# Kernel optimization log

Hardware: AMD Instinct MI355X
Metric: run time of the kernel (lower is better)

Reference implementation:

```python
import jax, jax.numpy as jnp
import numpy as np

N = 50000      # nodes
E = 800000     # edges
F_IN = 64      # num_node_features
H = 128        # hidden_channels
C = 2          # num_classes
G = 16         # graphs in batch


def setup_inputs() -> dict:
    key = jax.random.key(0)
    ks = jax.random.split(key, 16)
    def lin(k, fan_in, shape):
        return jax.random.normal(k, shape, jnp.float32) / np.sqrt(fan_in)
    return {
        "x": jax.random.normal(ks[0], (N, F_IN), jnp.float32),
        "edge_index": jax.random.randint(ks[1], (2, E), 0, N, dtype=jnp.int32),
        "batch": jnp.sort(jax.random.randint(ks[2], (N,), 0, G, dtype=jnp.int32)),
        "W1": lin(ks[3], F_IN, (F_IN, H)), "b1": jnp.zeros((H,), jnp.float32),
        "W2": lin(ks[4], H, (H, H)),       "b2": jnp.zeros((H,), jnp.float32),
        "W3": lin(ks[5], H, (H, H)),       "b3": jnp.zeros((H,), jnp.float32),
        "W4": lin(ks[6], H, (H, H)),       "b4": jnp.zeros((H,), jnp.float32),
        "lw1": lin(ks[7], H, (H, H // 2)), "lb1": jnp.zeros((H // 2,), jnp.float32),
        "lw2": lin(ks[8], H // 2, (H // 2, C)), "lb2": jnp.zeros((C,), jnp.float32),
    }


def _graph_norm(edge_index):
    # PyG GCNConv default: add self-loops, symmetric normalization.
    loop = jnp.arange(N, dtype=edge_index.dtype)
    src = jnp.concatenate([edge_index[0], loop])  # message source
    dst = jnp.concatenate([edge_index[1], loop])  # aggregation target
    deg = jax.ops.segment_sum(jnp.ones_like(dst, jnp.float32), dst, num_segments=N)
    dinv = jnp.where(deg > 0, jax.lax.rsqrt(deg), 0.0)
    norm = dinv[src] * dinv[dst]                  # [E+N]
    return src, dst, norm


def _gcn_conv(h, W, b, src, dst, norm):
    hw = h @ W                                    # [N, out]
    msg = hw[src] * norm[:, None]                 # gather + normalize  [E+N, out]
    agg = jax.ops.segment_sum(msg, dst, num_segments=N)  # scatter-add
    return agg + b


def reference(x, edge_index, batch, W1, b1, W2, b2, W3, b3, W4, b4, lw1, lb1, lw2, lb2):
    src, dst, norm = _graph_norm(edge_index)
    h = jax.nn.relu(_gcn_conv(x, W1, b1, src, dst, norm))   # dropout inactive (eval)
    h = jax.nn.relu(_gcn_conv(h, W2, b2, src, dst, norm))
    h = jax.nn.relu(_gcn_conv(h, W3, b3, src, dst, norm))
    h = _gcn_conv(h, W4, b4, src, dst, norm)
    # global_mean_pool over graph ids
    cnt = jax.ops.segment_sum(jnp.ones((N,), jnp.float32), batch, num_segments=G)
    pooled = jax.ops.segment_sum(h, batch, num_segments=G) / jnp.maximum(cnt, 1.0)[:, None]
    out = jax.nn.relu(pooled @ lw1 + lb1)
    return out @ lw2 + lb2
```

## Files before the change

### kernel.cpp

```cpp
#include <hip/hip_runtime.h>

#define NN 50000
#define NPAD 50048
#define NE 800000
#define FIN 64
#define H 128
#define NG 16
#define NPART 64
#define NBUCK 196
#define BUCK_CAP 4800
#define FILLA_BLOCKS 512
#define FILLA_CHUNK 1563
#define CHUNK_U 16
#define DUMMY NN
#define AGG_CH (NPAD / 64)
#define ZERO_I4 32768
#define PREP_ITEMS (NPAD * FIN + H * FIN + 3 * H * H + ZERO_I4)
#define PREP_BLOCKS ((PREP_ITEMS + 255) / 256)

typedef __bf16 bf16x8 __attribute__((ext_vector_type(8)));
typedef float f32x4 __attribute__((ext_vector_type(4)));
typedef float f32x2 __attribute__((ext_vector_type(2)));
typedef unsigned int u32x4 __attribute__((ext_vector_type(4)));

__device__ inline unsigned short bf16r(float x) {
    unsigned int u = __float_as_uint(x);
    return (unsigned short)((u + 0x7fffu + ((u >> 16) & 1u)) >> 16);
}
__device__ inline unsigned int pack_bf16x2(float a, float b) {
    return (unsigned int)bf16r(a) | ((unsigned int)bf16r(b) << 16);
}
__device__ inline float bf_lo(unsigned int u) { return __uint_as_float(u << 16); }
__device__ inline float bf_hi(unsigned int u) { return __uint_as_float(u & 0xffff0000u); }

__device__ inline void pkadd(f32x2& a, unsigned int u) {
    f32x2 p;
    p.x = bf_lo(u);
    p.y = bf_hi(u);
    asm("v_pk_add_f32 %0, %1, %0" : "+v"(a) : "v"(p));
}

__global__ __launch_bounds__(256) void fillA_prep_kernel(const int* __restrict__ ei,
                                                         int* __restrict__ gcount,
                                                         unsigned int* __restrict__ ebuf,
                                                         const float* __restrict__ x,
                                                         const float* __restrict__ W1,
                                                         const float* __restrict__ W2,
                                                         const float* __restrict__ W3,
                                                         const float* __restrict__ W4,
                                                         unsigned short* __restrict__ xb,
                                                         unsigned short* __restrict__ Wt1,
                                                         unsigned short* __restrict__ Wt2,
                                                         unsigned short* __restrict__ Wt3,
                                                         unsigned short* __restrict__ Wt4,
                                                         int4* __restrict__ zbuf) {
    const int t = threadIdx.x;
    if (blockIdx.x >= FILLA_BLOCKS) {
        int e = (blockIdx.x - FILLA_BLOCKS) * 256 + t;
        if (e < NPAD * FIN) {
            int n = e >> 6, k = e & 63;
            unsigned short v = (n < NN) ? bf16r(x[n * FIN + k]) : (unsigned short)0;
            xb[(size_t)(k >> 5) * (NPAD * 32) + n * 32 + (k & 31)] = v;
            return;
        }
        int tt = e - NPAD * FIN;
        if (tt < H * FIN) {
            int n = tt / FIN, k = tt % FIN;
            Wt1[tt] = bf16r(W1[k * H + n]);
            return;
        }
        int u = tt - H * FIN;
        if (u < 3 * H * H) {
            const float* W = W2;
            unsigned short* Wt = Wt2;
            if (u >= 2 * H * H) { W = W4; Wt = Wt4; u -= 2 * H * H; }
            else if (u >= H * H) { W = W3; Wt = Wt3; u -= H * H; }
            int n = u / H, k = u % H;
            Wt[u] = bf16r(W[k * H + n]);
            return;
        }
        int z = u - 3 * H * H;
        if (z < ZERO_I4) zbuf[z] = make_int4(0, 0, 0, 0);
        return;
    }
    __shared__ int hist[256];
    __shared__ int base[256];
    hist[t] = 0;
    __syncthreads();
    const int e0 = blockIdx.x * FILLA_CHUNK;
    const int e1 = min(e0 + FILLA_CHUNK, NE);
    for (int e = e0 + t; e < e1; e += 256)
        atomicAdd(&hist[ei[NE + e] >> 8], 1);
    __syncthreads();
    {
        int h = hist[t];
        base[t] = h ? atomicAdd(&gcount[t], h) : 0;
    }
    __syncthreads();
    for (int e = e0 + t; e < e1; e += 256) {
        int d = ei[NE + e];
        int s = ei[e];
        int b = d >> 8;
        int pos = atomicAdd(&base[b], 1);
        ebuf[b * BUCK_CAP + pos] = (unsigned int)s | ((unsigned int)d << 16);
    }
}

__global__ __launch_bounds__(256) void fillB_kernel(const unsigned int* __restrict__ ebuf,
                                                    const int* __restrict__ gcount,
                                                    int* __restrict__ galloc,
                                                    int* __restrict__ pcnt,
                                                    const int* __restrict__ batch,
                                                    int2* __restrict__ rowse,
                                                    float* __restrict__ dinv,
                                                    unsigned short* __restrict__ csr) {
    __shared__ int lh[256];
    __shared__ int lsum[256];
    __shared__ int lcur[256];
    __shared__ int lgc[16];
    __shared__ int base_s;
    const int b = blockIdx.x, t = threadIdx.x;
    const int n0 = b * 256;
    lh[t] = 0;
    if (t < 16) lgc[t] = 0;
    __syncthreads();
    const int ne = gcount[b];
    const unsigned int* __restrict__ eb = ebuf + b * BUCK_CAP;
    for (int i = t; i < ne; i += 256)
        atomicAdd(&lh[(int)(eb[i] >> 16) - n0], 1);
    __syncthreads();
    const int c = lh[t];
    const int p = (c + 7) & ~7;
    const int n = n0 + t;
    if (n < NN) atomicAdd(&lgc[batch[n]], 1);
    lsum[t] = p;
    __syncthreads();
    if (t < 16 && lgc[t]) atomicAdd(&pcnt[t], lgc[t]);
    for (int off = 1; off < 256; off <<= 1) {
        int u = (t >= off) ? lsum[t - off] : 0;
        __syncthreads();
        lsum[t] += u;
        __syncthreads();
    }
    if (t == 255) base_s = atomicAdd(galloc, lsum[255]);
    const int excl = t ? lsum[t - 1] : 0;
    __syncthreads();
    const int st = base_s + excl;
    if (n < NN) {
        rowse[n] = make_int2(st, st + p);
        dinv[n] = rsqrtf((float)c + 1.0f);
    } else if (n < NPAD) {
        rowse[n] = make_int2(0, 0);
        dinv[n] = 0.0f;
    }
    lcur[t] = st;
    __syncthreads();
    for (int i = t; i < ne; i += 256) {
        unsigned int u = eb[i];
        int pos = atomicAdd(&lcur[(int)(u >> 16) - n0], 1);
        csr[pos] = (unsigned short)(u & 0xFFFFu);
    }
    __syncthreads();
    for (int k = st + c; k < st + p; k++) csr[k] = (unsigned short)DUMMY;
}

#define LSTRIDE 130
template <int K>
__global__ __launch_bounds__(256) void gemm_mfma_kernel(const unsigned short* __restrict__ hb,
                                                        const unsigned short* __restrict__ Wt,
                                                        const float* __restrict__ dinv,
                                                        unsigned int* __restrict__ outu) {
    __shared__ float ls[64 * LSTRIDE];
    const int wave = threadIdx.x >> 6, lane = threadIdx.x & 63;
    const int m15 = lane & 15, quad = lane >> 4;
    const int row0 = blockIdx.x * 64;
    const int arow = row0 + wave * 16 + m15;

    bf16x8 a[K / 32];
#pragma unroll
    for (int ks = 0; ks < K / 32; ks++)
        a[ks] = *(const bf16x8*)&hb[(size_t)ks * (NPAD * 32) + arow * 32 + quad * 8];

    const int lrow = wave * 16 + quad * 4;
    float dv[4];
#pragma unroll
    for (int r = 0; r < 4; r++) dv[r] = dinv[row0 + lrow + r];

#pragma unroll
    for (int ct = 0; ct < 8; ct++) {
        f32x4 acc = {0.f, 0.f, 0.f, 0.f};
#pragma unroll
        for (int ks = 0; ks < K / 32; ks++) {
            bf16x8 b = *(const bf16x8*)&Wt[(ct * 16 + m15) * K + ks * 32 + quad * 8];
            acc = __builtin_amdgcn_mfma_f32_16x16x32_bf16(a[ks], b, acc, 0, 0, 0);
        }
#pragma unroll
        for (int r = 0; r < 4; r++)
            ls[(lrow + r) * LSTRIDE + ct * 16 + m15] = acc[r] * dv[r];
    }
    __syncthreads();

#pragma unroll
    for (int k = 0; k < 4; k++) {
        int idx = threadIdx.x + 256 * k;
        int c = idx >> 8, row = (idx >> 2) & 63, q = idx & 3;
        const float* p = &ls[row * LSTRIDE + c * 32 + q * 8];
        uint4 o;
        o.x = pack_bf16x2(p[0], p[1]);
        o.y = pack_bf16x2(p[2], p[3]);
        o.z = pack_bf16x2(p[4], p[5]);
        o.w = pack_bf16x2(p[6], p[7]);
        *(uint4*)&outu[(size_t)c * (NPAD * CHUNK_U) + (size_t)(row0 + row) * CHUNK_U + q * 4] = o;
    }
}

template <int MODE>
__global__ __launch_bounds__(256) void agg_kernel(const unsigned int* __restrict__ hwc,
                                                  const int2* __restrict__ rowse,
                                                  const unsigned short* __restrict__ csr,
                                                  const float* __restrict__ dinv,
                                                  const float* __restrict__ bias,
                                                  const int* __restrict__ batch,
                                                  float* __restrict__ poolpart,
                                                  unsigned int* __restrict__ outc) {
    const int b = blockIdx.x;
    const int chunk = (b & 7) >> 1;
    const int nb = (b >> 3) * 2 + (b & 1);
    const int g = threadIdx.x & 3;
    const int n = nb * 64 + (threadIdx.x >> 2);
    const int u0 = g * 4;
    const unsigned int* __restrict__ slice = hwc + (size_t)chunk * (NPAD * CHUNK_U);

    uint4 sv = *(const uint4*)&slice[n * CHUNK_U + u0];
    f32x2 a0 = {bf_lo(sv.x), bf_hi(sv.x)};
    f32x2 a1 = {bf_lo(sv.y), bf_hi(sv.y)};
    f32x2 a2 = {bf_lo(sv.z), bf_hi(sv.z)};
    f32x2 a3 = {bf_lo(sv.w), bf_hi(sv.w)};

    const int2 se = rowse[n];
    int i = se.x;
    for (; i + 16 <= se.y; i += 16) {
        uint4 c0 = *(const uint4*)&csr[i];
        uint4 c1 = *(const uint4*)&csr[i + 8];
        int s0 = c0.x & 0xFFFF, s1 = c0.x >> 16;
        int s2 = c0.y & 0xFFFF, s3 = c0.y >> 16;
        int s4 = c0.z & 0xFFFF, s5 = c0.z >> 16;
        int s6 = c0.w & 0xFFFF, s7 = c0.w >> 16;
        int t0 = c1.x & 0xFFFF, t1 = c1.x >> 16;
        int t2 = c1.y & 0xFFFF, t3 = c1.y >> 16;
        int t4 = c1.z & 0xFFFF, t5 = c1.z >> 16;
        int t6 = c1.w & 0xFFFF, t7 = c1.w >> 16;
        uint4 v0 = *(const uint4*)&slice[s0 * CHUNK_U + u0];
        uint4 v1 = *(const uint4*)&slice[s1 * CHUNK_U + u0];
        uint4 v2 = *(const uint4*)&slice[s2 * CHUNK_U + u0];
        uint4 v3 = *(const uint4*)&slice[s3 * CHUNK_U + u0];
        uint4 v4 = *(const uint4*)&slice[s4 * CHUNK_U + u0];
        uint4 v5 = *(const uint4*)&slice[s5 * CHUNK_U + u0];
        uint4 v6 = *(const uint4*)&slice[s6 * CHUNK_U + u0];
        uint4 v7 = *(const uint4*)&slice[s7 * CHUNK_U + u0];
        uint4 w0 = *(const uint4*)&slice[t0 * CHUNK_U + u0];
        uint4 w1 = *(const uint4*)&slice[t1 * CHUNK_U + u0];
        uint4 w2 = *(const uint4*)&slice[t2 * CHUNK_U + u0];
        uint4 w3 = *(const uint4*)&slice[t3 * CHUNK_U + u0];
        uint4 w4 = *(const uint4*)&slice[t4 * CHUNK_U + u0];
        uint4 w5 = *(const uint4*)&slice[t5 * CHUNK_U + u0];
        uint4 w6 = *(const uint4*)&slice[t6 * CHUNK_U + u0];
        uint4 w7 = *(const uint4*)&slice[t7 * CHUNK_U + u0];
        pkadd(a0, v0.x); pkadd(a1, v0.y); pkadd(a2, v0.z); pkadd(a3, v0.w);
        pkadd(a0, v1.x); pkadd(a1, v1.y); pkadd(a2, v1.z); pkadd(a3, v1.w);
        pkadd(a0, v2.x); pkadd(a1, v2.y); pkadd(a2, v2.z); pkadd(a3, v2.w);
        pkadd(a0, v3.x); pkadd(a1, v3.y); pkadd(a2, v3.z); pkadd(a3, v3.w);
        pkadd(a0, v4.x); pkadd(a1, v4.y); pkadd(a2, v4.z); pkadd(a3, v4.w);
        pkadd(a0, v5.x); pkadd(a1, v5.y); pkadd(a2, v5.z); pkadd(a3, v5.w);
        pkadd(a0, v6.x); pkadd(a1, v6.y); pkadd(a2, v6.z); pkadd(a3, v6.w);
        pkadd(a0, v7.x); pkadd(a1, v7.y); pkadd(a2, v7.z); pkadd(a3, v7.w);
        pkadd(a0, w0.x); pkadd(a1, w0.y); pkadd(a2, w0.z); pkadd(a3, w0.w);
        pkadd(a0, w1.x); pkadd(a1, w1.y); pkadd(a2, w1.z); pkadd(a3, w1.w);
        pkadd(a0, w2.x); pkadd(a1, w2.y); pkadd(a2, w2.z); pkadd(a3, w2.w);
        pkadd(a0, w3.x); pkadd(a1, w3.y); pkadd(a2, w3.z); pkadd(a3, w3.w);
        pkadd(a0, w4.x); pkadd(a1, w4.y); pkadd(a2, w4.z); pkadd(a3, w4.w);
        pkadd(a0, w5.x); pkadd(a1, w5.y); pkadd(a2, w5.z); pkadd(a3, w5.w);
        pkadd(a0, w6.x); pkadd(a1, w6.y); pkadd(a2, w6.z); pkadd(a3, w6.w);
        pkadd(a0, w7.x); pkadd(a1, w7.y); pkadd(a2, w7.z); pkadd(a3, w7.w);
    }
    if (i < se.y) {
        uint4 c = *(const uint4*)&csr[i];
        int s0 = c.x & 0xFFFF, s1 = c.x >> 16;
        int s2 = c.y & 0xFFFF, s3 = c.y >> 16;
        int s4 = c.z & 0xFFFF, s5 = c.z >> 16;
        int s6 = c.w & 0xFFFF, s7 = c.w >> 16;
        uint4 v0 = *(const uint4*)&slice[s0 * CHUNK_U + u0];
        uint4 v1 = *(const uint4*)&slice[s1 * CHUNK_U + u0];
        uint4 v2 = *(const uint4*)&slice[s2 * CHUNK_U + u0];
        uint4 v3 = *(const uint4*)&slice[s3 * CHUNK_U + u0];
        uint4 v4 = *(const uint4*)&slice[s4 * CHUNK_U + u0];
        uint4 v5 = *(const uint4*)&slice[s5 * CHUNK_U + u0];
        uint4 v6 = *(const uint4*)&slice[s6 * CHUNK_U + u0];
        uint4 v7 = *(const uint4*)&slice[s7 * CHUNK_U + u0];
        pkadd(a0, v0.x); pkadd(a1, v0.y); pkadd(a2, v0.z); pkadd(a3, v0.w);
        pkadd(a0, v1.x); pkadd(a1, v1.y); pkadd(a2, v1.z); pkadd(a3, v1.w);
        pkadd(a0, v2.x); pkadd(a1, v2.y); pkadd(a2, v2.z); pkadd(a3, v2.w);
        pkadd(a0, v3.x); pkadd(a1, v3.y); pkadd(a2, v3.z); pkadd(a3, v3.w);
        pkadd(a0, v4.x); pkadd(a1, v4.y); pkadd(a2, v4.z); pkadd(a3, v4.w);
        pkadd(a0, v5.x); pkadd(a1, v5.y); pkadd(a2, v5.z); pkadd(a3, v5.w);
        pkadd(a0, v6.x); pkadd(a1, v6.y); pkadd(a2, v6.z); pkadd(a3, v6.w);
        pkadd(a0, v7.x); pkadd(a1, v7.y); pkadd(a2, v7.z); pkadd(a3, v7.w);
    }

    const float d = dinv[n];
    if (MODE == 1) {
        a0 *= d; a1 *= d; a2 *= d; a3 *= d;
        const int lane = threadIdx.x & 63;
        const int wv = threadIdx.x >> 6;
        const int gb = batch[min(n, NN - 1)];
        const int gfirst = __shfl(gb, 0);
        const bool uni = (__shfl(gb, 63) == gfirst);
        float* __restrict__ pp = poolpart + (((b << 2) + wv) & (NPART - 1)) * (NG * H);
        if (uni) {
#pragma unroll
            for (int m = 4; m <= 32; m <<= 1) {
                a0.x += __shfl_xor(a0.x, m); a0.y += __shfl_xor(a0.y, m);
                a1.x += __shfl_xor(a1.x, m); a1.y += __shfl_xor(a1.y, m);
                a2.x += __shfl_xor(a2.x, m); a2.y += __shfl_xor(a2.y, m);
                a3.x += __shfl_xor(a3.x, m); a3.y += __shfl_xor(a3.y, m);
            }
            if (lane < 4) {
                float* q = pp + gfirst * H + chunk * 32 + lane * 8;
                atomicAdd(&q[0], a0.x); atomicAdd(&q[1], a0.y);
                atomicAdd(&q[2], a1.x); atomicAdd(&q[3], a1.y);
                atomicAdd(&q[4], a2.x); atomicAdd(&q[5], a2.y);
                atomicAdd(&q[6], a3.x); atomicAdd(&q[7], a3.y);
            }
        } else if (n < NN) {
            float* q = pp + gb * H + chunk * 32 + g * 8;
            atomicAdd(&q[0], a0.x); atomicAdd(&q[1], a0.y);
            atomicAdd(&q[2], a1.x); atomicAdd(&q[3], a1.y);
            atomicAdd(&q[4], a2.x); atomicAdd(&q[5], a2.y);
            atomicAdd(&q[6], a3.x); atomicAdd(&q[7], a3.y);
        }
        return;
    }
    const float2* bp = (const float2*)bias + chunk * CHUNK_U + u0;
    float2 q0 = bp[0], q1 = bp[1], q2 = bp[2], q3 = bp[3];
    u32x4 o;
    o[0] = pack_bf16x2(fmaxf(a0.x * d + q0.x, 0.f), fmaxf(a0.y * d + q0.y, 0.f));
    o[1] = pack_bf16x2(fmaxf(a1.x * d + q1.x, 0.f), fmaxf(a1.y * d + q1.y, 0.f));
    o[2] = pack_bf16x2(fmaxf(a2.x * d + q2.x, 0.f), fmaxf(a2.y * d + q2.y, 0.f));
    o[3] = pack_bf16x2(fmaxf(a3.x * d + q3.x, 0.f), fmaxf(a3.y * d + q3.y, 0.f));
    __builtin_nontemporal_store(
        o, (u32x4*)&outc[(size_t)chunk * (NPAD * CHUNK_U) + (size_t)n * CHUNK_U + u0]);
}

__global__ __launch_bounds__(1024) void mlp_kernel(const float* __restrict__ poolpart,
                                                   const int* __restrict__ pcnt,
                                                   const float* __restrict__ b4,
                                                   const float* __restrict__ lw1,
                                                   const float* __restrict__ lb1,
                                                   const float* __restrict__ lw2,
                                                   const float* __restrict__ lb2,
                                                   float* __restrict__ out) {
    __shared__ float mean_s[NG * H];
    __shared__ float cnt_s[NG];
    __shared__ float hid_s[NG * 64];
    int tid = threadIdx.x;
    if (tid < NG) cnt_s[tid] = fmaxf((float)pcnt[tid], 1.0f);
    __syncthreads();
    for (int i = tid; i < NG * H; i += 1024) {
        float s = 0.f;
        for (int p = 0; p < NPART; p++) s += poolpart[p * (NG * H) + i];
        mean_s[i] = s / cnt_s[i >> 7] + b4[i & (H - 1)];
    }
    __syncthreads();
    {
        int g = tid >> 6, j = tid & 63;
        float acc = lb1[j];
        for (int f = 0; f < H; f++) acc += mean_s[g * H + f] * lw1[f * 64 + j];
        hid_s[g * 64 + j] = fmaxf(acc, 0.f);
    }
    __syncthreads();
    if (tid < 32) {
        int g = tid >> 1, c = tid & 1;
        float acc = lb2[c];
        for (int j = 0; j < 64; j++) acc += hid_s[g * 64 + j] * lw2[j * 2 + c];
        out[g * 2 + c] = acc;
    }
}

extern "C" void kernel_launch(void* const* d_in, const int* in_sizes, int n_in,
                              void* d_out, int out_size, void* d_ws, size_t ws_size,
                              hipStream_t stream) {
    const float* x = (const float*)d_in[0];
    const int* ei = (const int*)d_in[1];
    const int* batch = (const int*)d_in[2];
    const float* W1 = (const float*)d_in[3];
    const float* b1 = (const float*)d_in[4];
    const float* W2 = (const float*)d_in[5];
    const float* b2 = (const float*)d_in[6];
    const float* W3 = (const float*)d_in[7];
    const float* b3 = (const float*)d_in[8];
    const float* W4 = (const float*)d_in[9];
    const float* b4 = (const float*)d_in[10];
    const float* lw1 = (const float*)d_in[11];
    const float* lb1 = (const float*)d_in[12];
    const float* lw2 = (const float*)d_in[13];
    const float* lb2 = (const float*)d_in[14];
    float* out = (float*)d_out;

    int* wsi = (int*)d_ws;
    int* gcount = wsi;
    int* galloc = wsi + 256;
    int* pcnt = wsi + 280;
    float* poolpart = (float*)(wsi + 512);
    int2* rowse = (int2*)(wsi + 131584);
    unsigned short* csr = (unsigned short*)(wsi + 231680);
    float* dinv = (float*)(wsi + 831680);
    unsigned short* Wt1 = (unsigned short*)(wsi + 881728);
    unsigned short* Wt2 = (unsigned short*)(wsi + 885824);
    unsigned short* Wt3 = (unsigned short*)(wsi + 894016);
    unsigned short* Wt4 = (unsigned short*)(wsi + 902208);
    unsigned short* xb = (unsigned short*)(wsi + 910400);
    unsigned int* hb = (unsigned int*)(wsi + 2511936);
    unsigned int* hwb = (unsigned int*)(wsi + 5715008);
    unsigned int* ebuf = (unsigned int*)(wsi + 8918080);

    const int gemmBlocks = NPAD / 64;
    const int aggBlocks = 4 * AGG_CH;

    hipMemsetAsync(wsi, 0, 512 * sizeof(int), stream);
    fillA_prep_kernel<<<FILLA_BLOCKS + PREP_BLOCKS, 256, 0, stream>>>(
        ei, gcount, ebuf, x, W1, W2, W3, W4, xb, Wt1, Wt2, Wt3, Wt4, (int4*)poolpart);
    fillB_kernel<<<NBUCK, 256, 0, stream>>>(ebuf, gcount, galloc, pcnt, batch,
                                            rowse, dinv, csr);

    gemm_mfma_kernel<FIN><<<gemmBlocks, 256, 0, stream>>>(xb, Wt1, dinv, hwb);
    agg_kernel<0><<<aggBlocks, 256, 0, stream>>>(hwb, rowse, csr, dinv, b1, batch,
                                                 nullptr, hb);
    gemm_mfma_kernel<H><<<gemmBlocks, 256, 0, stream>>>((unsigned short*)hb, Wt2, dinv, hwb);
    agg_kernel<0><<<aggBlocks, 256, 0, stream>>>(hwb, rowse, csr, dinv, b2, batch,
                                                 nullptr, hb);
    gemm_mfma_kernel<H><<<gemmBlocks, 256, 0, stream>>>((unsigned short*)hb, Wt3, dinv, hwb);
    agg_kernel<0><<<aggBlocks, 256, 0, stream>>>(hwb, rowse, csr, dinv, b3, batch,
                                                 nullptr, hb);
    gemm_mfma_kernel<H><<<gemmBlocks, 256, 0, stream>>>((unsigned short*)hb, Wt4, dinv, hwb);
    agg_kernel<1><<<aggBlocks, 256, 0, stream>>>(hwb, rowse, csr, dinv, nullptr, batch,
                                                 poolpart, nullptr);

    mlp_kernel<<<1, 1024, 0, stream>>>(poolpart, pcnt, b4, lw1, lb1, lw2, lb2, out);
}
```

Before: 318.4 us.

## Split hidden features into eight 16-column chunks for gather-aggregation locality

Changes the chunked feature layout from four 32-column slices to eight 16-column slices. Each aggregation block now handles one slice over 128 nodes with two threads per node, so each gathered neighbor row is a single 32-byte segment and the per-slice working set is smaller and more cache-resident. The GEMM gains an input-layout template flag to read the new layout, and it now writes its output with nontemporal stores. The CSR index loads in aggregation also become nontemporal. In exchange, each CSR row is read by twice as many blocks and pooling reductions use one more shuffle step.

Measured after the change: 394.2 us. +23.8%, slower.

```diff
diff --git a/kernel.cpp b/kernel.cpp
--- a/kernel.cpp
+++ b/kernel.cpp
@@ -11,9 +11,9 @@
 #define BUCK_CAP 4800
 #define FILLA_BLOCKS 512
 #define FILLA_CHUNK 1563
-#define CHUNK_U 16
+#define CHUNK_U 8
 #define DUMMY NN
-#define AGG_CH (NPAD / 64)
+#define AGG_NB (NPAD / 128)
 #define ZERO_I4 32768
 #define PREP_ITEMS (NPAD * FIN + H * FIN + 3 * H * H + ZERO_I4)
 #define PREP_BLOCKS ((PREP_ITEMS + 255) / 256)
@@ -165,7 +165,7 @@
 }
 
 #define LSTRIDE 130
-template <int K>
+template <int K, bool IN8>
 __global__ __launch_bounds__(256) void gemm_mfma_kernel(const unsigned short* __restrict__ hb,
                                                         const unsigned short* __restrict__ Wt,
                                                         const float* __restrict__ dinv,
@@ -178,8 +178,13 @@
 
     bf16x8 a[K / 32];
 #pragma unroll
-    for (int ks = 0; ks < K / 32; ks++)
-        a[ks] = *(const bf16x8*)&hb[(size_t)ks * (NPAD * 32) + arow * 32 + quad * 8];
+    for (int ks = 0; ks < K / 32; ks++) {
+        if (IN8)
+            a[ks] = *(const bf16x8*)&hb[(size_t)(ks * 2 + (quad >> 1)) * (NPAD * 16) +
+                                        arow * 16 + (quad & 1) * 8];
+        else
+            a[ks] = *(const bf16x8*)&hb[(size_t)ks * (NPAD * 32) + arow * 32 + quad * 8];
+    }
 
     const int lrow = wave * 16 + quad * 4;
     float dv[4];
@@ -203,14 +208,16 @@
 #pragma unroll
     for (int k = 0; k < 4; k++) {
         int idx = threadIdx.x + 256 * k;
-        int c = idx >> 8, row = (idx >> 2) & 63, q = idx & 3;
-        const float* p = &ls[row * LSTRIDE + c * 32 + q * 8];
-        uint4 o;
-        o.x = pack_bf16x2(p[0], p[1]);
-        o.y = pack_bf16x2(p[2], p[3]);
-        o.z = pack_bf16x2(p[4], p[5]);
-        o.w = pack_bf16x2(p[6], p[7]);
-        *(uint4*)&outu[(size_t)c * (NPAD * CHUNK_U) + (size_t)(row0 + row) * CHUNK_U + q * 4] = o;
+        int c = idx >> 7, row = (idx >> 1) & 63, q = idx & 1;
+        const float* p = &ls[row * LSTRIDE + c * 16 + q * 8];
+        u32x4 o;
+        o[0] = pack_bf16x2(p[0], p[1]);
+        o[1] = pack_bf16x2(p[2], p[3]);
+        o[2] = pack_bf16x2(p[4], p[5]);
+        o[3] = pack_bf16x2(p[6], p[7]);
+        __builtin_nontemporal_store(
+            o, (u32x4*)&outu[(size_t)c * (NPAD * CHUNK_U) +
+                             (size_t)(row0 + row) * CHUNK_U + q * 4]);
     }
 }
 
@@ -224,11 +231,10 @@
                                                   float* __restrict__ poolpart,
                                                   unsigned int* __restrict__ outc) {
     const int b = blockIdx.x;
-    const int chunk = (b & 7) >> 1;
-    const int nb = (b >> 3) * 2 + (b & 1);
-    const int g = threadIdx.x & 3;
-    const int n = nb * 64 + (threadIdx.x >> 2);
-    const int u0 = g * 4;
+    const int chunk = b & 7;
+    const int nb = b >> 3;
+    const int n = nb * 128 + (threadIdx.x >> 1);
+    const int u0 = (threadIdx.x & 1) * 4;
     const unsigned int* __restrict__ slice = hwc + (size_t)chunk * (NPAD * CHUNK_U);
 
     uint4 sv = *(const uint4*)&slice[n * CHUNK_U + u0];
@@ -240,16 +246,16 @@
     const int2 se = rowse[n];
     int i = se.x;
     for (; i + 16 <= se.y; i += 16) {
-        uint4 c0 = *(const uint4*)&csr[i];
-        uint4 c1 = *(const uint4*)&csr[i + 8];
-        int s0 = c0.x & 0xFFFF, s1 = c0.x >> 16;
-        int s2 = c0.y & 0xFFFF, s3 = c0.y >> 16;
-        int s4 = c0.z & 0xFFFF, s5 = c0.z >> 16;
-        int s6 = c0.w & 0xFFFF, s7 = c0.w >> 16;
-        int t0 = c1.x & 0xFFFF, t1 = c1.x >> 16;
-        int t2 = c1.y & 0xFFFF, t3 = c1.y >> 16;
-        int t4 = c1.z & 0xFFFF, t5 = c1.z >> 16;
-        int t6 = c1.w & 0xFFFF, t7 = c1.w >> 16;
+        u32x4 c0 = __builtin_nontemporal_load((const u32x4*)&csr[i]);
+        u32x4 c1 = __builtin_nontemporal_load((const u32x4*)&csr[i + 8]);
+        int s0 = c0[0] & 0xFFFF, s1 = c0[0] >> 16;
+        int s2 = c0[1] & 0xFFFF, s3 = c0[1] >> 16;
+        int s4 = c0[2] & 0xFFFF, s5 = c0[2] >> 16;
+        int s6 = c0[3] & 0xFFFF, s7 = c0[3] >> 16;
+        int t0 = c1[0] & 0xFFFF, t1 = c1[0] >> 16;
+        int t2 = c1[1] & 0xFFFF, t3 = c1[1] >> 16;
+        int t4 = c1[2] & 0xFFFF, t5 = c1[2] >> 16;
+        int t6 = c1[3] & 0xFFFF, t7 = c1[3] >> 16;
         uint4 v0 = *(const uint4*)&slice[s0 * CHUNK_U + u0];
         uint4 v1 = *(const uint4*)&slice[s1 * CHUNK_U + u0];
         uint4 v2 = *(const uint4*)&slice[s2 * CHUNK_U + u0];
@@ -284,11 +290,11 @@
         pkadd(a0, w7.x); pkadd(a1, w7.y); pkadd(a2, w7.z); pkadd(a3, w7.w);
     }
     if (i < se.y) {
-        uint4 c = *(const uint4*)&csr[i];
-        int s0 = c.x & 0xFFFF, s1 = c.x >> 16;
-        int s2 = c.y & 0xFFFF, s3 = c.y >> 16;
-        int s4 = c.z & 0xFFFF, s5 = c.z >> 16;
-        int s6 = c.w & 0xFFFF, s7 = c.w >> 16;
+        u32x4 c = __builtin_nontemporal_load((const u32x4*)&csr[i]);
+        int s0 = c[0] & 0xFFFF, s1 = c[0] >> 16;
+        int s2 = c[1] & 0xFFFF, s3 = c[1] >> 16;
+        int s4 = c[2] & 0xFFFF, s5 = c[2] >> 16;
+        int s6 = c[3] & 0xFFFF, s7 = c[3] >> 16;
         uint4 v0 = *(const uint4*)&slice[s0 * CHUNK_U + u0];
         uint4 v1 = *(const uint4*)&slice[s1 * CHUNK_U + u0];
         uint4 v2 = *(const uint4*)&slice[s2 * CHUNK_U + u0];
@@ -318,21 +324,21 @@
         float* __restrict__ pp = poolpart + (((b << 2) + wv) & (NPART - 1)) * (NG * H);
         if (uni) {
 #pragma unroll
-            for (int m = 4; m <= 32; m <<= 1) {
+            for (int m = 2; m <= 32; m <<= 1) {
                 a0.x += __shfl_xor(a0.x, m); a0.y += __shfl_xor(a0.y, m);
                 a1.x += __shfl_xor(a1.x, m); a1.y += __shfl_xor(a1.y, m);
                 a2.x += __shfl_xor(a2.x, m); a2.y += __shfl_xor(a2.y, m);
                 a3.x += __shfl_xor(a3.x, m); a3.y += __shfl_xor(a3.y, m);
             }
-            if (lane < 4) {
-                float* q = pp + gfirst * H + chunk * 32 + lane * 8;
+            if (lane < 2) {
+                float* q = pp + gfirst * H + chunk * 16 + lane * 8;
                 atomicAdd(&q[0], a0.x); atomicAdd(&q[1], a0.y);
                 atomicAdd(&q[2], a1.x); atomicAdd(&q[3], a1.y);
                 atomicAdd(&q[4], a2.x); atomicAdd(&q[5], a2.y);
                 atomicAdd(&q[6], a3.x); atomicAdd(&q[7], a3.y);
             }
         } else if (n < NN) {
-            float* q = pp + gb * H + chunk * 32 + g * 8;
+            float* q = pp + gb * H + chunk * 16 + (threadIdx.x & 1) * 8;
             atomicAdd(&q[0], a0.x); atomicAdd(&q[1], a0.y);
             atomicAdd(&q[2], a1.x); atomicAdd(&q[3], a1.y);
             atomicAdd(&q[4], a2.x); atomicAdd(&q[5], a2.y);
@@ -424,7 +430,7 @@
     unsigned int* ebuf = (unsigned int*)(wsi + 8918080);
 
     const int gemmBlocks = NPAD / 64;
-    const int aggBlocks = 4 * AGG_CH;
+    const int aggBlocks = 8 * AGG_NB;
 
     hipMemsetAsync(wsi, 0, 512 * sizeof(int), stream);
     fillA_prep_kernel<<<FILLA_BLOCKS + PREP_BLOCKS, 256, 0, stream>>>(
@@ -432,16 +438,19 @@
     fillB_kernel<<<NBUCK, 256, 0, stream>>>(ebuf, gcount, galloc, pcnt, batch,
                                             rowse, dinv, csr);
 
-    gemm_mfma_kernel<FIN><<<gemmBlocks, 256, 0, stream>>>(xb, Wt1, dinv, hwb);
+    gemm_mfma_kernel<FIN, false><<<gemmBlocks, 256, 0, stream>>>(xb, Wt1, dinv, hwb);
     agg_kernel<0><<<aggBlocks, 256, 0, stream>>>(hwb, rowse, csr, dinv, b1, batch,
                                                  nullptr, hb);
-    gemm_mfma_kernel<H><<<gemmBlocks, 256, 0, stream>>>((unsigned short*)hb, Wt2, dinv, hwb);
+    gemm_mfma_kernel<H, true><<<gemmBlocks, 256, 0, stream>>>((unsigned short*)hb, Wt2,
+                                                              dinv, hwb);
     agg_kernel<0><<<aggBlocks, 256, 0, stream>>>(hwb, rowse, csr, dinv, b2, batch,
                                                  nullptr, hb);
-    gemm_mfma_kernel<H><<<gemmBlocks, 256, 0, stream>>>((unsigned short*)hb, Wt3, dinv, hwb);
+    gemm_mfma_kernel<H, true><<<gemmBlocks, 256, 0, stream>>>((unsigned short*)hb, Wt3,
+                                                              dinv, hwb);
     agg_kernel<0><<<aggBlocks, 256, 0, stream>>>(hwb, rowse, csr, dinv, b3, batch,
                                                  nullptr, hb);
-    gemm_mfma_kernel<H><<<gemmBlocks, 256, 0, stream>>>((unsigned short*)hb, Wt4, dinv, hwb);
+    gemm_mfma_kernel<H, true><<<gemmBlocks, 256, 0, stream>>>((unsigned short*)hb, Wt4,
+                                                              dinv, hwb);
     agg_kernel<1><<<aggBlocks, 256, 0, stream>>>(hwb, rowse, csr, dinv, nullptr, batch,
                                                  poolpart, nullptr);
 
```
